# Kernel tuning notes

Hardware: AMD Instinct MI355X
Metric: run time of the kernel (lower is better)

## Reference

```python
import jax, jax.numpy as jnp
import numpy as np

N_NODES = 100000
N_EDGES = 1600000
N_GRAPHS = 2000
N_FEAT = 128
HIDDEN = 128
N_LAYERS = 4
BN_EPS = 1e-5


def setup_inputs() -> dict:
    key = jax.random.key(0)
    ks = jax.random.split(key, 8)
    x = jax.random.normal(ks[0], (N_NODES, N_FEAT), dtype=jnp.float32)
    edge_index = jax.random.randint(ks[1], (2, N_EDGES), 0, N_NODES, dtype=jnp.int32)
    batch = jnp.sort(jax.random.randint(ks[2], (N_NODES,), 0, N_GRAPHS, dtype=jnp.int32))
    # layer weights scaled down to keep activations stable over 4 layers
    Ws = jax.random.normal(ks[3], (N_LAYERS, HIDDEN, HIDDEN), dtype=jnp.float32) * 0.1
    bs = jnp.zeros((N_LAYERS, HIDDEN), jnp.float32)
    gammas = jnp.ones((N_LAYERS, HIDDEN), jnp.float32)
    betas = jnp.zeros((N_LAYERS, HIDDEN), jnp.float32)
    run_mean = jnp.zeros((N_LAYERS, HIDDEN), jnp.float32)
    run_var = jnp.ones((N_LAYERS, HIDDEN), jnp.float32)
    W_out = jax.random.normal(ks[4], (HIDDEN, 5), dtype=jnp.float32) * 0.1
    b_out = jnp.zeros((5,), jnp.float32)
    return {"x": x, "edge_index": edge_index, "batch": batch, "Ws": Ws, "bs": bs,
            "gammas": gammas, "betas": betas, "run_mean": run_mean, "run_var": run_var,
            "W_out": W_out, "b_out": b_out}


def _gcn_conv(x, src, dst, norm, self_coef, W, b):
    xw = x @ W                                        # [N, H]
    coef = norm[src] * norm[dst]                      # [E]
    msgs = xw[src] * coef[:, None]                    # [E, H] gather
    agg = jax.ops.segment_sum(msgs, dst, num_segments=N_NODES)  # scatter-add
    agg = agg + xw * self_coef[:, None]               # self-loop term
    return agg + b


def reference(x, edge_index, batch, Ws, bs, gammas, betas, run_mean, run_var, W_out, b_out):
    src, dst = edge_index[0], edge_index[1]
    # degree (incl. self-loop) from destination index
    deg = jax.ops.segment_sum(jnp.ones((N_EDGES,), x.dtype), dst, num_segments=N_NODES) + 1.0
    norm = jax.lax.rsqrt(deg)
    self_coef = norm * norm
    h = x
    for l in range(N_LAYERS):
        h = _gcn_conv(h, src, dst, norm, self_coef, Ws[l], bs[l])
        # BatchNorm1d in eval mode (running stats); dropout is identity in eval
        h = (h - run_mean[l]) * (gammas[l] * jax.lax.rsqrt(run_var[l] + BN_EPS)) + betas[l]
        h = jax.nn.relu(h)
    # global mean pool over graphs
    sums = jax.ops.segment_sum(h, batch, num_segments=N_GRAPHS)
    counts = jax.ops.segment_sum(jnp.ones((N_NODES,), h.dtype), batch, num_segments=N_GRAPHS)
    pooled = sums / jnp.maximum(counts, 1.0)[:, None]  # [G, H]
    return pooled @ W_out + b_out                      # [G, 5]
```

## Files before the change

kernel.cpp:

```cpp
#include <hip/hip_runtime.h>
#include <hip/hip_fp16.h>

#define N_NODES_C 100000
#define N_EDGES_C 1600000
#define N_GRAPHS_C 2000
#define HID 128
#define BN_EPS_C 1e-5f
#define NBUCK 391
#define PART_TILE 4096

typedef _Float16 half8 __attribute__((ext_vector_type(8)));
typedef float float4v __attribute__((ext_vector_type(4)));


__global__ __launch_bounds__(256) void kb_hist(const int* __restrict__ dst, int* __restrict__ bcount) {
    __shared__ int hist[NBUCK];
    const int t = threadIdx.x;
    for (int b = t; b < NBUCK; b += 256) hist[b] = 0;
    __syncthreads();
    const int e0 = blockIdx.x * PART_TILE;
    #pragma unroll
    for (int k = 0; k < 16; k++) {
        int e = e0 + k * 256 + t;
        if (e < N_EDGES_C) atomicAdd(&hist[dst[e] >> 8], 1);
    }
    __syncthreads();
    for (int b = t; b < NBUCK; b += 256) {
        int c = hist[b];
        if (c) atomicAdd(&bcount[b], c);
    }
}

__global__ __launch_bounds__(512) void kb_scan(const int* __restrict__ bcount,
                                               int* __restrict__ bbase, int* __restrict__ bcursor) {
    __shared__ int s[512];
    const int t = threadIdx.x;
    int v = (t < NBUCK) ? bcount[t] : 0;
    s[t] = v;
    __syncthreads();
    for (int off = 1; off < 512; off <<= 1) {
        int u = (t >= off) ? s[t - off] : 0;
        __syncthreads();
        s[t] += u;
        __syncthreads();
    }
    if (t < NBUCK) { int e = s[t] - v; bbase[t] = e; bcursor[t] = e; }
    if (t == 0) bbase[NBUCK] = N_EDGES_C;
}

__global__ __launch_bounds__(256) void kb_part(const int* __restrict__ src, const int* __restrict__ dst,
                                               int* __restrict__ bcursor, int2* __restrict__ ebuf) {
    __shared__ int hist[NBUCK];
    __shared__ int startA[NBUCK];
    __shared__ int lcur[NBUCK];
    const int t = threadIdx.x;
    for (int b = t; b < NBUCK; b += 256) { hist[b] = 0; lcur[b] = 0; }
    __syncthreads();
    const int e0 = blockIdx.x * PART_TILE;
    #pragma unroll
    for (int k = 0; k < 16; k++) {
        int e = e0 + k * 256 + t;
        if (e < N_EDGES_C) atomicAdd(&hist[dst[e] >> 8], 1);
    }
    __syncthreads();
    for (int b = t; b < NBUCK; b += 256) {
        int c = hist[b];
        startA[b] = c ? atomicAdd(&bcursor[b], c) : 0;
    }
    __syncthreads();
    #pragma unroll
    for (int k = 0; k < 16; k++) {
        int e = e0 + k * 256 + t;
        if (e < N_EDGES_C) {
            int d = dst[e];
            int b = d >> 8;
            int pos = startA[b] + atomicAdd(&lcur[b], 1);
            ebuf[pos] = make_int2(src[e], d);
        }
    }
}

__global__ __launch_bounds__(256) void kb_fill(const int2* __restrict__ ebuf, const int* __restrict__ bbase,
                                               int* __restrict__ csr_src, int* __restrict__ offs,
                                               float* __restrict__ norm) {
    __shared__ int s[256];
    __shared__ int excl[256];
    __shared__ int lcur[256];
    const int b = blockIdx.x, t = threadIdx.x;
    const int base = b << 8;
    const int e0 = bbase[b], e1 = bbase[b + 1];
    s[t] = 0; lcur[t] = 0;
    __syncthreads();
    for (int e = e0 + t; e < e1; e += 256)
        atomicAdd(&s[ebuf[e].y & 255], 1);
    __syncthreads();
    int own = s[t];
    for (int off = 1; off < 256; off <<= 1) {
        int v = (t >= off) ? s[t - off] : 0;
        __syncthreads();
        s[t] += v;
        __syncthreads();
    }
    excl[t] = s[t] - own;
    int node = base + t;
    if (node < N_NODES_C) {
        offs[node] = e0 + (s[t] - own);
        norm[node] = rsqrtf((float)own + 1.0f);
    }
    if (b == 0 && t == 0) offs[N_NODES_C] = N_EDGES_C;
    __syncthreads();
    for (int e = e0 + t; e < e1; e += 256) {
        int2 p = ebuf[e];
        int l = p.y & 255;
        int pos = e0 + excl[l] + atomicAdd(&lcur[l], 1);
        csr_src[pos] = p.x;
    }
}


__global__ __launch_bounds__(256) void k_cast(const float* __restrict__ x, _Float16* __restrict__ xh) {
    long i = ((long)blockIdx.x * 256 + threadIdx.x) * 8;
    float4 a = *(const float4*)&x[i];
    float4 b = *(const float4*)&x[i + 4];
    _Float16 p[8] = {(_Float16)a.x, (_Float16)a.y, (_Float16)a.z, (_Float16)a.w,
                     (_Float16)b.x, (_Float16)b.y, (_Float16)b.z, (_Float16)b.w};
    *(half8*)&xh[i] = *(half8*)p;
}

__global__ __launch_bounds__(256) void k_tw(const float* __restrict__ Ws_all, _Float16* __restrict__ WT) {
    int idx = blockIdx.x * 256 + threadIdx.x;
    int l = idx >> 14, r = idx & 16383, k = r >> 7, n = r & 127;
    WT[l * 16384 + n * HID + k] = (_Float16)Ws_all[idx];
}


__global__ __launch_bounds__(256) void k_gemm(const _Float16* __restrict__ Ah,
                                              const _Float16* __restrict__ WT,
                                              const float* __restrict__ norm,
                                              _Float16* __restrict__ Y, int nrows) {
    __shared__ _Float16 Wt[HID][136];
    const int tid = threadIdx.x;
    #pragma unroll
    for (int t = 0; t < 8; t++) {
        int off = tid * 8 + t * 2048;
        half8 v = *(const half8*)&WT[off];
        *(half8*)&Wt[off >> 7][off & 127] = v;
    }
    __syncthreads();

    const int wave = tid >> 6, lane = tid & 63, quad = lane >> 4, l16 = lane & 15;
    half8 Wf[2][4];
    #pragma unroll
    for (int c = 0; c < 2; c++)
        #pragma unroll
        for (int ks = 0; ks < 4; ks++)
            Wf[c][ks] = *(const half8*)&Wt[(wave * 2 + c) * 16 + l16][ks * 32 + quad * 8];

    const int nbase = blockIdx.x * 128;
    #pragma unroll
    for (int t = 0; t < 8; t++) {
        int node = nbase + t * 16 + l16;
        bool ok = node < nrows;
        half8 Af[4];
        const _Float16* arow = Ah + (long)node * HID;
        #pragma unroll
        for (int ks = 0; ks < 4; ks++)
            Af[ks] = ok ? *(const half8*)&arow[ks * 32 + quad * 8] : half8{};
        float4v a0 = {0.f, 0.f, 0.f, 0.f}, a1 = {0.f, 0.f, 0.f, 0.f};
        #pragma unroll
        for (int ks = 0; ks < 4; ks++) {
            a0 = __builtin_amdgcn_mfma_f32_16x16x32_f16(Wf[0][ks], Af[ks], a0, 0, 0, 0);
            a1 = __builtin_amdgcn_mfma_f32_16x16x32_f16(Wf[1][ks], Af[ks], a1, 0, 0, 0);
        }
        if (ok) {
            float nv = norm[node];
            _Float16 p0[4], p1[4];
            #pragma unroll
            for (int r = 0; r < 4; r++) {
                p0[r] = (_Float16)(a0[r] * nv);
                p1[r] = (_Float16)(a1[r] * nv);
            }
            *(ushort4*)&Y[(long)node * HID + (wave * 2 + 0) * 16 + quad * 4] = *(ushort4*)p0;
            *(ushort4*)&Y[(long)node * HID + (wave * 2 + 1) * 16 + quad * 4] = *(ushort4*)p1;
        }
    }
}


__global__ __launch_bounds__(256) void k_agg(const __half* __restrict__ y, const int* __restrict__ offs,
                                             const int* __restrict__ csr_src, const float* __restrict__ norm,
                                             const float* __restrict__ bias, const float* __restrict__ mean,
                                             const float* __restrict__ gamma, const float* __restrict__ var,
                                             const float* __restrict__ beta, __half* __restrict__ h) {
    const int wave = __builtin_amdgcn_readfirstlane(threadIdx.x >> 6);
    const int lane = threadIdx.x & 63;
    const int i = blockIdx.x * 4 + wave;
    const int j = lane * 2;

    float2 f = __half22float2(*(const __half2*)&y[(long)i * HID + j]);
    float acc0 = f.x, acc1 = f.y;

    const int e0 = offs[i], e1 = offs[i + 1];
    int e = e0;
    #define GATHER(EE) { \
        int s_ = csr_src[EE]; \
        float2 g_ = __half22float2(*(const __half2*)&y[(long)s_ * HID + j]); \
        acc0 += g_.x; acc1 += g_.y; }
    for (; e + 8 <= e1; e += 8) {
        GATHER(e) GATHER(e + 1) GATHER(e + 2) GATHER(e + 3)
        GATHER(e + 4) GATHER(e + 5) GATHER(e + 6) GATHER(e + 7)
    }
    for (; e < e1; e++) GATHER(e)
    #undef GATHER

    float ni = norm[i];
    float2 bi = *(const float2*)&bias[j];
    float2 me = *(const float2*)&mean[j];
    float2 ga = *(const float2*)&gamma[j];
    float2 va = *(const float2*)&var[j];
    float2 be = *(const float2*)&beta[j];
    float v0 = (acc0 * ni + bi.x - me.x) * (ga.x * rsqrtf(va.x + BN_EPS_C)) + be.x;
    float v1 = (acc1 * ni + bi.y - me.y) * (ga.y * rsqrtf(va.y + BN_EPS_C)) + be.y;
    *(__half2*)&h[(long)i * HID + j] = __floats2half2_rn(fmaxf(v0, 0.f), fmaxf(v1, 0.f));
}


__global__ __launch_bounds__(128) void k_pool(const __half* __restrict__ h, const int* __restrict__ batch,
                                              float* __restrict__ psum, int* __restrict__ pcount) {
    const int j = threadIdx.x;
    const int i0 = blockIdx.x * 128;
    const int iend = min(i0 + 128, N_NODES_C);
    if (i0 >= N_NODES_C) return;
    float acc = 0.f;
    int cur = batch[i0];
    int runStart = i0;
    for (int i = i0; i < iend; i++) {
        int g = batch[i];
        if (g != cur) {
            atomicAdd(&psum[(long)cur * HID + j], acc);
            if (j == 0) atomicAdd(&pcount[cur], i - runStart);
            acc = 0.f; cur = g; runStart = i;
        }
        acc += __half2float(h[(long)i * HID + j]);
    }
    atomicAdd(&psum[(long)cur * HID + j], acc);
    if (j == 0) atomicAdd(&pcount[cur], iend - runStart);
}

__global__ __launch_bounds__(128) void k_final(const float* __restrict__ psum, const int* __restrict__ pcount,
                                               const float* __restrict__ W_out, const float* __restrict__ b_out,
                                               float* __restrict__ out) {
    __shared__ float red[128][5];
    const int g = blockIdx.x, j = threadIdx.x;
    float cnt = fmaxf((float)pcount[g], 1.f);
    float p = psum[(long)g * HID + j] / cnt;
    #pragma unroll
    for (int o = 0; o < 5; o++) red[j][o] = p * W_out[j * 5 + o];
    __syncthreads();
    for (int off = 64; off >= 1; off >>= 1) {
        if (j < off) {
            #pragma unroll
            for (int o = 0; o < 5; o++) red[j][o] += red[j + off][o];
        }
        __syncthreads();
    }
    if (j < 5) out[g * 5 + j] = red[0][j] + b_out[j];
}


extern "C" void kernel_launch(void* const* d_in, const int* in_sizes, int n_in,
                              void* d_out, int out_size, void* d_ws, size_t ws_size,
                              hipStream_t stream) {
    const float* x        = (const float*)d_in[0];
    const int*   eidx     = (const int*)d_in[1];
    const int*   src      = eidx;
    const int*   dst      = eidx + N_EDGES_C;
    const int*   batch    = (const int*)d_in[2];
    const float* Ws_all   = (const float*)d_in[3];
    const float* bs       = (const float*)d_in[4];
    const float* gammas   = (const float*)d_in[5];
    const float* betas    = (const float*)d_in[6];
    const float* run_mean = (const float*)d_in[7];
    const float* run_var  = (const float*)d_in[8];
    const float* W_out    = (const float*)d_in[9];
    const float* b_out    = (const float*)d_in[10];
    float* out = (float*)d_out;

    char* wp = (char*)d_ws;
    auto alloc = [&](size_t bytes) { char* p = wp; wp += (bytes + 255) & ~(size_t)255; return p; };
    __half*   h       = (__half*)alloc((size_t)N_NODES_C * HID * 2);
    _Float16* y       = (_Float16*)alloc((size_t)N_NODES_C * HID * 2);
    int2*     ebuf    = (int2*)y;
    _Float16* xh      = (_Float16*)alloc((size_t)N_NODES_C * HID * 2);
    _Float16* WT      = (_Float16*)alloc((size_t)4 * HID * HID * 2);
    int*      csr_src = (int*)alloc((size_t)N_EDGES_C * 4);
    int*      offs    = (int*)alloc((size_t)(N_NODES_C + 1) * 4);
    float*    norm    = (float*)alloc((size_t)N_NODES_C * 4);
    int*      bcount  = (int*)alloc((NBUCK + 1) * 4);
    int*      bbase   = (int*)alloc((NBUCK + 1) * 4);
    int*      bcursor = (int*)alloc((NBUCK + 1) * 4);
    float*    psum    = (float*)alloc((size_t)N_GRAPHS_C * HID * 4);
    int*      pcount  = (int*)alloc((size_t)N_GRAPHS_C * 4);

    hipMemsetAsync(bcount, 0, (NBUCK + 1) * 4, stream);
    hipMemsetAsync(psum,   0, (size_t)N_GRAPHS_C * HID * 4, stream);
    hipMemsetAsync(pcount, 0, (size_t)N_GRAPHS_C * 4, stream);

    k_cast<<<(N_NODES_C * HID) / 2048, 256, 0, stream>>>(x, xh);
    k_tw  <<<256, 256, 0, stream>>>(Ws_all, WT);

    const int PB = (N_EDGES_C + PART_TILE - 1) / PART_TILE;
    kb_hist<<<PB, 256, 0, stream>>>(dst, bcount);
    kb_scan<<<1, 512, 0, stream>>>(bcount, bbase, bcursor);
    kb_part<<<PB, 256, 0, stream>>>(src, dst, bcursor, ebuf);
    kb_fill<<<NBUCK, 256, 0, stream>>>(ebuf, bbase, csr_src, offs, norm);

    const int GB = (N_NODES_C + 127) / 128;
    const int AB = (N_NODES_C + 3) / 4;
    for (int l = 0; l < 4; l++) {
        const _Float16* A = (l == 0) ? xh : (const _Float16*)h;
        k_gemm<<<GB, 256, 0, stream>>>(A, WT + (size_t)l * HID * HID, norm, y, N_NODES_C);
        k_agg<<<AB, 256, 0, stream>>>((const __half*)y, offs, csr_src, norm,
                                      bs + l * HID, run_mean + l * HID, gammas + l * HID,
                                      run_var + l * HID, betas + l * HID, h);
    }
    k_pool <<<GB, 128, 0, stream>>>(h, batch, psum, pcount);
    k_final<<<N_GRAPHS_C, 128, 0, stream>>>(psum, pcount, W_out, b_out, out);
}
```

Before: 555.5 us.

## Fuse aggregation and GEMM into one per-layer kernel using aggregate-then-transform

Reorders each GCN layer to aggregate the pre-scaled features first and then multiply by W, so gather and MFMA GEMM run in one kernel through a shared-memory tile. The norm scaling moves into the previous layer's epilogue and into the input cast, and the BN constants are precomputed once. The edge buffer packs the source index and the low byte of dst into a single 32-bit word. This removes one kernel launch and one full feature round-trip per layer. In exchange, each block does its gather serially across only 4 waves, which risks poor latency hiding and lower occupancy.

```diff
diff --git a/kernel.cpp b/kernel.cpp
--- a/kernel.cpp
+++ b/kernel.cpp
@@ -10,6 +10,7 @@
 #define PART_TILE 4096
 
 typedef _Float16 half8 __attribute__((ext_vector_type(8)));
+typedef _Float16 half4v __attribute__((ext_vector_type(4)));
 typedef float float4v __attribute__((ext_vector_type(4)));
 
 
@@ -49,7 +50,7 @@
 }
 
 __global__ __launch_bounds__(256) void kb_part(const int* __restrict__ src, const int* __restrict__ dst,
-                                               int* __restrict__ bcursor, int2* __restrict__ ebuf) {
+                                               int* __restrict__ bcursor, unsigned int* __restrict__ ebuf) {
     __shared__ int hist[NBUCK];
     __shared__ int startA[NBUCK];
     __shared__ int lcur[NBUCK];
@@ -75,12 +76,12 @@
             int d = dst[e];
             int b = d >> 8;
             int pos = startA[b] + atomicAdd(&lcur[b], 1);
-            ebuf[pos] = make_int2(src[e], d);
-        }
-    }
-}
-
-__global__ __launch_bounds__(256) void kb_fill(const int2* __restrict__ ebuf, const int* __restrict__ bbase,
+            ebuf[pos] = ((unsigned int)src[e] << 8) | (unsigned int)(d & 255);
+        }
+    }
+}
+
+__global__ __launch_bounds__(256) void kb_fill(const unsigned int* __restrict__ ebuf, const int* __restrict__ bbase,
                                                int* __restrict__ csr_src, int* __restrict__ offs,
                                                float* __restrict__ norm) {
     __shared__ int s[256];
@@ -92,7 +93,7 @@
     s[t] = 0; lcur[t] = 0;
     __syncthreads();
     for (int e = e0 + t; e < e1; e += 256)
-        atomicAdd(&s[ebuf[e].y & 255], 1);
+        atomicAdd(&s[ebuf[e] & 255u], 1);
     __syncthreads();
     int own = s[t];
     for (int off = 1; off < 256; off <<= 1) {
@@ -110,21 +111,24 @@
     if (b == 0 && t == 0) offs[N_NODES_C] = N_EDGES_C;
     __syncthreads();
     for (int e = e0 + t; e < e1; e += 256) {
-        int2 p = ebuf[e];
-        int l = p.y & 255;
+        unsigned int p = ebuf[e];
+        int l = p & 255u;
         int pos = e0 + excl[l] + atomicAdd(&lcur[l], 1);
-        csr_src[pos] = p.x;
-    }
-}
-
-
-__global__ __launch_bounds__(256) void k_cast(const float* __restrict__ x, _Float16* __restrict__ xh) {
-    long i = ((long)blockIdx.x * 256 + threadIdx.x) * 8;
-    float4 a = *(const float4*)&x[i];
-    float4 b = *(const float4*)&x[i + 4];
-    _Float16 p[8] = {(_Float16)a.x, (_Float16)a.y, (_Float16)a.z, (_Float16)a.w,
-                     (_Float16)b.x, (_Float16)b.y, (_Float16)b.z, (_Float16)b.w};
-    *(half8*)&xh[i] = *(half8*)p;
+        csr_src[pos] = (int)(p >> 8);
+    }
+}
+
+
+__global__ __launch_bounds__(256) void k_cast(const float* __restrict__ x, const float* __restrict__ norm,
+                                              _Float16* __restrict__ xh) {
+    long base = ((long)blockIdx.x * 256 + threadIdx.x) * 8;
+    int row = (int)(base >> 7);
+    float nv = norm[row];
+    float4 a = *(const float4*)&x[base];
+    float4 b = *(const float4*)&x[base + 4];
+    _Float16 p[8] = {(_Float16)(a.x * nv), (_Float16)(a.y * nv), (_Float16)(a.z * nv), (_Float16)(a.w * nv),
+                     (_Float16)(b.x * nv), (_Float16)(b.y * nv), (_Float16)(b.z * nv), (_Float16)(b.w * nv)};
+    *(half8*)&xh[base] = *(half8*)p;
 }
 
 __global__ __launch_bounds__(256) void k_tw(const float* __restrict__ Ws_all, _Float16* __restrict__ WT) {
@@ -133,117 +137,149 @@
     WT[l * 16384 + n * HID + k] = (_Float16)Ws_all[idx];
 }
 
-
-__global__ __launch_bounds__(256) void k_gemm(const _Float16* __restrict__ Ah,
-                                              const _Float16* __restrict__ WT,
-                                              const float* __restrict__ norm,
-                                              _Float16* __restrict__ Y, int nrows) {
-    __shared__ _Float16 Wt[HID][136];
+__global__ __launch_bounds__(256) void k_bn(const float* __restrict__ bs, const float* __restrict__ mean,
+                                            const float* __restrict__ gamma, const float* __restrict__ var,
+                                            const float* __restrict__ beta,
+                                            float* __restrict__ Asc, float* __restrict__ Bsh) {
+    int i = blockIdx.x * 256 + threadIdx.x;
+    if (i < 4 * HID) {
+        float sc = gamma[i] * rsqrtf(var[i] + BN_EPS_C);
+        Asc[i] = sc;
+        Bsh[i] = (bs[i] - mean[i]) * sc + beta[i];
+    }
+}
+
+
+__global__ __launch_bounds__(256, 4) void k_layer(const _Float16* __restrict__ hin,
+                                                  const _Float16* __restrict__ WT,
+                                                  const int* __restrict__ offs, const int* __restrict__ csr_src,
+                                                  const float* __restrict__ norm,
+                                                  const float* __restrict__ Asc, const float* __restrict__ Bsh,
+                                                  _Float16* __restrict__ hout, int scale_out) {
+    __shared__ _Float16 g[128][136];
     const int tid = threadIdx.x;
-    #pragma unroll
-    for (int t = 0; t < 8; t++) {
-        int off = tid * 8 + t * 2048;
-        half8 v = *(const half8*)&WT[off];
-        *(half8*)&Wt[off >> 7][off & 127] = v;
-    }
-    __syncthreads();
-
-    const int wave = tid >> 6, lane = tid & 63, quad = lane >> 4, l16 = lane & 15;
+    const int wave = tid >> 6, lane = tid & 63;
+    const int quad = lane >> 4, l16 = lane & 15;
+    const int half = lane >> 5, cl = lane & 31;
+    const int nbase = blockIdx.x * 128;
+
     half8 Wf[2][4];
     #pragma unroll
     for (int c = 0; c < 2; c++)
         #pragma unroll
         for (int ks = 0; ks < 4; ks++)
-            Wf[c][ks] = *(const half8*)&Wt[(wave * 2 + c) * 16 + l16][ks * 32 + quad * 8];
-
-    const int nbase = blockIdx.x * 128;
+            Wf[c][ks] = *(const half8*)&WT[((wave * 2 + c) * 16 + l16) * HID + ks * 32 + quad * 8];
+
+    for (int t = 0; t < 32; t++) {
+        const int local = wave * 32 + t;
+        const int node = nbase + local;
+        if (node < N_NODES_C) {
+            float nv = norm[node];
+            float acc[4] = {0.f, 0.f, 0.f, 0.f};
+            if (half == 0) {
+                half4v sv = *(const half4v*)&hin[(long)node * HID + cl * 4];
+                #pragma unroll
+                for (int r = 0; r < 4; r++) acc[r] += (float)sv[r];
+            }
+            const int e0 = offs[node], e1 = offs[node + 1];
+            int e = e0;
+            for (; e + 8 <= e1; e += 8) {
+                int s0 = csr_src[e + half];
+                int s1 = csr_src[e + 2 + half];
+                int s2 = csr_src[e + 4 + half];
+                int s3 = csr_src[e + 6 + half];
+                half4v v0 = *(const half4v*)&hin[(long)s0 * HID + cl * 4];
+                half4v v1 = *(const half4v*)&hin[(long)s1 * HID + cl * 4];
+                half4v v2 = *(const half4v*)&hin[(long)s2 * HID + cl * 4];
+                half4v v3 = *(const half4v*)&hin[(long)s3 * HID + cl * 4];
+                #pragma unroll
+                for (int r = 0; r < 4; r++)
+                    acc[r] += (float)v0[r] + (float)v1[r] + (float)v2[r] + (float)v3[r];
+            }
+            for (; e + 2 <= e1; e += 2) {
+                int s = csr_src[e + half];
+                half4v v = *(const half4v*)&hin[(long)s * HID + cl * 4];
+                #pragma unroll
+                for (int r = 0; r < 4; r++) acc[r] += (float)v[r];
+            }
+            if (e + half < e1) {
+                int s = csr_src[e + half];
+                half4v v = *(const half4v*)&hin[(long)s * HID + cl * 4];
+                #pragma unroll
+                for (int r = 0; r < 4; r++) acc[r] += (float)v[r];
+            }
+            #pragma unroll
+            for (int r = 0; r < 4; r++) acc[r] += __shfl_xor(acc[r], 32);
+            if (half == 0) {
+                _Float16 p[4];
+                #pragma unroll
+                for (int r = 0; r < 4; r++) p[r] = (_Float16)(nv * acc[r]);
+                *(ushort4*)&g[local][cl * 4] = *(ushort4*)p;
+            }
+        } else if (half == 0) {
+            ushort4 z = make_ushort4(0, 0, 0, 0);
+            *(ushort4*)&g[local][cl * 4] = z;
+        }
+    }
+    __syncthreads();
+
+    float4 A0 = *(const float4*)&Asc[(wave * 2 + 0) * 16 + quad * 4];
+    float4 A1 = *(const float4*)&Asc[(wave * 2 + 1) * 16 + quad * 4];
+    float4 B0 = *(const float4*)&Bsh[(wave * 2 + 0) * 16 + quad * 4];
+    float4 B1 = *(const float4*)&Bsh[(wave * 2 + 1) * 16 + quad * 4];
     #pragma unroll
     for (int t = 0; t < 8; t++) {
-        int node = nbase + t * 16 + l16;
-        bool ok = node < nrows;
-        half8 Af[4];
-        const _Float16* arow = Ah + (long)node * HID;
+        half8 Bf[4];
         #pragma unroll
         for (int ks = 0; ks < 4; ks++)
-            Af[ks] = ok ? *(const half8*)&arow[ks * 32 + quad * 8] : half8{};
+            Bf[ks] = *(const half8*)&g[t * 16 + l16][ks * 32 + quad * 8];
         float4v a0 = {0.f, 0.f, 0.f, 0.f}, a1 = {0.f, 0.f, 0.f, 0.f};
         #pragma unroll
         for (int ks = 0; ks < 4; ks++) {
-            a0 = __builtin_amdgcn_mfma_f32_16x16x32_f16(Wf[0][ks], Af[ks], a0, 0, 0, 0);
-            a1 = __builtin_amdgcn_mfma_f32_16x16x32_f16(Wf[1][ks], Af[ks], a1, 0, 0, 0);
-        }
-        if (ok) {
-            float nv = norm[node];
+            a0 = __builtin_amdgcn_mfma_f32_16x16x32_f16(Wf[0][ks], Bf[ks], a0, 0, 0, 0);
+            a1 = __builtin_amdgcn_mfma_f32_16x16x32_f16(Wf[1][ks], Bf[ks], a1, 0, 0, 0);
+        }
+        int node = nbase + t * 16 + l16;
+        if (node < N_NODES_C) {
+            float nv = scale_out ? norm[node] : 1.0f;
             _Float16 p0[4], p1[4];
-            #pragma unroll
-            for (int r = 0; r < 4; r++) {
-                p0[r] = (_Float16)(a0[r] * nv);
-                p1[r] = (_Float16)(a1[r] * nv);
-            }
-            *(ushort4*)&Y[(long)node * HID + (wave * 2 + 0) * 16 + quad * 4] = *(ushort4*)p0;
-            *(ushort4*)&Y[(long)node * HID + (wave * 2 + 1) * 16 + quad * 4] = *(ushort4*)p1;
-        }
-    }
-}
-
-
-__global__ __launch_bounds__(256) void k_agg(const __half* __restrict__ y, const int* __restrict__ offs,
-                                             const int* __restrict__ csr_src, const float* __restrict__ norm,
-                                             const float* __restrict__ bias, const float* __restrict__ mean,
-                                             const float* __restrict__ gamma, const float* __restrict__ var,
-                                             const float* __restrict__ beta, __half* __restrict__ h) {
-    const int wave = __builtin_amdgcn_readfirstlane(threadIdx.x >> 6);
-    const int lane = threadIdx.x & 63;
-    const int i = blockIdx.x * 4 + wave;
-    const int j = lane * 2;
-
-    float2 f = __half22float2(*(const __half2*)&y[(long)i * HID + j]);
-    float acc0 = f.x, acc1 = f.y;
-
-    const int e0 = offs[i], e1 = offs[i + 1];
-    int e = e0;
-    #define GATHER(EE) { \
-        int s_ = csr_src[EE]; \
-        float2 g_ = __half22float2(*(const __half2*)&y[(long)s_ * HID + j]); \
-        acc0 += g_.x; acc1 += g_.y; }
-    for (; e + 8 <= e1; e += 8) {
-        GATHER(e) GATHER(e + 1) GATHER(e + 2) GATHER(e + 3)
-        GATHER(e + 4) GATHER(e + 5) GATHER(e + 6) GATHER(e + 7)
-    }
-    for (; e < e1; e++) GATHER(e)
-    #undef GATHER
-
-    float ni = norm[i];
-    float2 bi = *(const float2*)&bias[j];
-    float2 me = *(const float2*)&mean[j];
-    float2 ga = *(const float2*)&gamma[j];
-    float2 va = *(const float2*)&var[j];
-    float2 be = *(const float2*)&beta[j];
-    float v0 = (acc0 * ni + bi.x - me.x) * (ga.x * rsqrtf(va.x + BN_EPS_C)) + be.x;
-    float v1 = (acc1 * ni + bi.y - me.y) * (ga.y * rsqrtf(va.y + BN_EPS_C)) + be.y;
-    *(__half2*)&h[(long)i * HID + j] = __floats2half2_rn(fmaxf(v0, 0.f), fmaxf(v1, 0.f));
-}
-
-
-__global__ __launch_bounds__(128) void k_pool(const __half* __restrict__ h, const int* __restrict__ batch,
-                                              float* __restrict__ psum, int* __restrict__ pcount) {
+            p0[0] = (_Float16)(fmaxf(a0[0] * A0.x + B0.x, 0.f) * nv);
+            p0[1] = (_Float16)(fmaxf(a0[1] * A0.y + B0.y, 0.f) * nv);
+            p0[2] = (_Float16)(fmaxf(a0[2] * A0.z + B0.z, 0.f) * nv);
+            p0[3] = (_Float16)(fmaxf(a0[3] * A0.w + B0.w, 0.f) * nv);
+            p1[0] = (_Float16)(fmaxf(a1[0] * A1.x + B1.x, 0.f) * nv);
+            p1[1] = (_Float16)(fmaxf(a1[1] * A1.y + B1.y, 0.f) * nv);
+            p1[2] = (_Float16)(fmaxf(a1[2] * A1.z + B1.z, 0.f) * nv);
+            p1[3] = (_Float16)(fmaxf(a1[3] * A1.w + B1.w, 0.f) * nv);
+            *(ushort4*)&hout[(long)node * HID + (wave * 2 + 0) * 16 + quad * 4] = *(ushort4*)p0;
+            *(ushort4*)&hout[(long)node * HID + (wave * 2 + 1) * 16 + quad * 4] = *(ushort4*)p1;
+        }
+    }
+}
+
+
+__global__ __launch_bounds__(64) void k_pool(const __half* __restrict__ h, const int* __restrict__ batch,
+                                             float* __restrict__ psum, int* __restrict__ pcount) {
     const int j = threadIdx.x;
     const int i0 = blockIdx.x * 128;
     const int iend = min(i0 + 128, N_NODES_C);
     if (i0 >= N_NODES_C) return;
-    float acc = 0.f;
+    float acc0 = 0.f, acc1 = 0.f;
     int cur = batch[i0];
     int runStart = i0;
     for (int i = i0; i < iend; i++) {
-        int g = batch[i];
-        if (g != cur) {
-            atomicAdd(&psum[(long)cur * HID + j], acc);
+        int gidx = batch[i];
+        if (gidx != cur) {
+            atomicAdd(&psum[(long)cur * HID + 2 * j], acc0);
+            atomicAdd(&psum[(long)cur * HID + 2 * j + 1], acc1);
             if (j == 0) atomicAdd(&pcount[cur], i - runStart);
-            acc = 0.f; cur = g; runStart = i;
-        }
-        acc += __half2float(h[(long)i * HID + j]);
-    }
-    atomicAdd(&psum[(long)cur * HID + j], acc);
+            acc0 = 0.f; acc1 = 0.f; cur = gidx; runStart = i;
+        }
+        float2 f = __half22float2(*(const __half2*)&h[(long)i * HID + 2 * j]);
+        acc0 += f.x; acc1 += f.y;
+    }
+    atomicAdd(&psum[(long)cur * HID + 2 * j], acc0);
+    atomicAdd(&psum[(long)cur * HID + 2 * j + 1], acc1);
     if (j == 0) atomicAdd(&pcount[cur], iend - runStart);
 }
 
@@ -288,11 +324,12 @@
 
     char* wp = (char*)d_ws;
     auto alloc = [&](size_t bytes) { char* p = wp; wp += (bytes + 255) & ~(size_t)255; return p; };
-    __half*   h       = (__half*)alloc((size_t)N_NODES_C * HID * 2);
-    _Float16* y       = (_Float16*)alloc((size_t)N_NODES_C * HID * 2);
-    int2*     ebuf    = (int2*)y;
-    _Float16* xh      = (_Float16*)alloc((size_t)N_NODES_C * HID * 2);
+    _Float16* hA      = (_Float16*)alloc((size_t)N_NODES_C * HID * 2);
+    _Float16* hB      = (_Float16*)alloc((size_t)N_NODES_C * HID * 2);
+    unsigned int* ebuf = (unsigned int*)hB;
     _Float16* WT      = (_Float16*)alloc((size_t)4 * HID * HID * 2);
+    float*    Asc     = (float*)alloc((size_t)4 * HID * 4);
+    float*    Bsh     = (float*)alloc((size_t)4 * HID * 4);
     int*      csr_src = (int*)alloc((size_t)N_EDGES_C * 4);
     int*      offs    = (int*)alloc((size_t)(N_NODES_C + 1) * 4);
     float*    norm    = (float*)alloc((size_t)N_NODES_C * 4);
@@ -306,24 +343,24 @@
     hipMemsetAsync(psum,   0, (size_t)N_GRAPHS_C * HID * 4, stream);
     hipMemsetAsync(pcount, 0, (size_t)N_GRAPHS_C * 4, stream);
 
-    k_cast<<<(N_NODES_C * HID) / 2048, 256, 0, stream>>>(x, xh);
-    k_tw  <<<256, 256, 0, stream>>>(Ws_all, WT);
-
     const int PB = (N_EDGES_C + PART_TILE - 1) / PART_TILE;
     kb_hist<<<PB, 256, 0, stream>>>(dst, bcount);
     kb_scan<<<1, 512, 0, stream>>>(bcount, bbase, bcursor);
     kb_part<<<PB, 256, 0, stream>>>(src, dst, bcursor, ebuf);
     kb_fill<<<NBUCK, 256, 0, stream>>>(ebuf, bbase, csr_src, offs, norm);
 
-    const int GB = (N_NODES_C + 127) / 128;
-    const int AB = (N_NODES_C + 3) / 4;
+    k_tw  <<<256, 256, 0, stream>>>(Ws_all, WT);
+    k_bn  <<<2, 256, 0, stream>>>(bs, run_mean, gammas, run_var, betas, Asc, Bsh);
+    k_cast<<<(N_NODES_C * HID) / 2048, 256, 0, stream>>>(x, norm, hA);
+
+    const int LB = (N_NODES_C + 127) / 128;
+    _Float16* bufs[2] = {hA, hB};
     for (int l = 0; l < 4; l++) {
-        const _Float16* A = (l == 0) ? xh : (const _Float16*)h;
-        k_gemm<<<GB, 256, 0, stream>>>(A, WT + (size_t)l * HID * HID, norm, y, N_NODES_C);
-        k_agg<<<AB, 256, 0, stream>>>((const __half*)y, offs, csr_src, norm,
-                                      bs + l * HID, run_mean + l * HID, gammas + l * HID,
-                                      run_var + l * HID, betas + l * HID, h);
-    }
-    k_pool <<<GB, 128, 0, stream>>>(h, batch, psum, pcount);
+        k_layer<<<LB, 256, 0, stream>>>(bufs[l & 1], WT + (size_t)l * HID * HID,
+                                        offs, csr_src, norm,
+                                        Asc + l * HID, Bsh + l * HID,
+                                        bufs[(l + 1) & 1], (l < 3) ? 1 : 0);
+    }
+    k_pool <<<LB, 64, 0, stream>>>((const __half*)bufs[0], batch, psum, pcount);
     k_final<<<N_GRAPHS_C, 128, 0, stream>>>(psum, pcount, W_out, b_out, out);
 }
```

Measured after the change: 713.1 us. +28.4%, slower.
